# Optimization experiments

Measured on AMD Instinct MI355X. Metric: run time of the kernel, lower is better.

Reference implementation:

```python
import jax, jax.numpy as jnp
import numpy as np
import math

B, T, D_IN, D_OUT = 2, 2048, 4096, 4096
N_HEADS, N_KV = 32, 8
HEAD_DIM = D_OUT // N_HEADS  # 128
GROUP_SIZE = N_HEADS // N_KV  # 4
ROPE_BASE = 500000.0
CTX = 2048


def _rope_tables(head_dim, base, seq_len):
    inv_freq = 1.0 / base ** (jnp.arange(0, head_dim, 2, dtype=jnp.float32) / head_dim)
    t = jnp.arange(seq_len, dtype=jnp.float32)
    freqs = jnp.einsum('i,j->ij', t, inv_freq)  # (T, head_dim/2)
    return jnp.cos(freqs), jnp.sin(freqs)


def _apply_rope(x, cos, sin):
    # x: (B, H, T, Dh); cos/sin: (T, Dh/2)
    x1, x2 = jnp.split(x, 2, axis=-1)
    c = cos[None, None]
    s = sin[None, None]
    return jnp.concatenate([x1 * c - x2 * s, x1 * s + x2 * c], axis=-1)


def setup_inputs() -> dict:
    key = jax.random.key(0)
    ks = jax.random.split(key, 5)
    scale = 0.02
    return {
        'x': jax.random.normal(ks[0], (B, T, D_IN), dtype=jnp.float32),
        'Wq': jax.random.normal(ks[1], (D_IN, D_OUT), dtype=jnp.float32) * scale,
        'Wk': jax.random.normal(ks[2], (D_IN, N_KV * HEAD_DIM), dtype=jnp.float32) * scale,
        'Wv': jax.random.normal(ks[3], (D_IN, N_KV * HEAD_DIM), dtype=jnp.float32) * scale,
        'Wo': jax.random.normal(ks[4], (D_OUT, D_OUT), dtype=jnp.float32) * scale,
    }


def reference(x, Wq, Wk, Wv, Wo):
    b, t, _ = x.shape
    cos, sin = _rope_tables(HEAD_DIM, ROPE_BASE, t)  # start_pos = 0

    q = (x @ Wq).reshape(b, t, N_HEADS, HEAD_DIM).transpose(0, 2, 1, 3)  # (B,H,T,Dh)
    k = (x @ Wk).reshape(b, t, N_KV, HEAD_DIM).transpose(0, 2, 1, 3)    # (B,G,T,Dh)
    v = (x @ Wv).reshape(b, t, N_KV, HEAD_DIM).transpose(0, 2, 1, 3)    # (B,G,T,Dh)

    q = _apply_rope(q, cos, sin)
    k = _apply_rope(k, cos, sin)

    # GQA: repeat_interleave KV groups to match query heads
    k_h = jnp.repeat(k, GROUP_SIZE, axis=1)  # (B,H,T,Dh)
    v_h = jnp.repeat(v, GROUP_SIZE, axis=1)

    scores = jnp.einsum('bhqd,bhkd->bhqk', q, k_h) / math.sqrt(HEAD_DIM)
    causal = jnp.triu(jnp.ones((t, t), dtype=bool), k=1)
    scores = jnp.where(causal[None, None], jnp.finfo(scores.dtype).min, scores)
    attn = jax.nn.softmax(scores, axis=-1)

    ctx = jnp.einsum('bhqk,bhkd->bhqd', attn, v_h)           # (B,H,T,Dh)
    ctx = ctx.transpose(0, 2, 1, 3).reshape(b, t, D_OUT)     # (B,T,D)
    return ctx @ Wo
```

## Files before the change

kernel.cpp:

```cpp
#include <hip/hip_runtime.h>
#include <hip/hip_bf16.h>

#define T_SEQ 2048
#define NH 32
#define NKV 8
#define DH 128

typedef unsigned short u16;
typedef unsigned int u32;
typedef __attribute__((ext_vector_type(8))) short short8;
typedef __attribute__((ext_vector_type(4))) float floatx4;

union U8 { u16 s[8]; uint4 v; };
union F8 { u32 d[4]; short8 s; };

__device__ inline u16 f2bf(float f) {
  __hip_bfloat16 h = __float2bfloat16(f);
  return *reinterpret_cast<u16*>(&h);
}
__device__ inline float bf2f(u16 u) {
  __hip_bfloat16 h;
  *reinterpret_cast<u16*>(&h) = u;
  return __bfloat162float(h);
}

__device__ inline void store_out(float* p, float v) { *p = v; }
__device__ inline void store_out(u16* p, float v) { *p = f2bf(v); }

#define GLD_LDS(g, l) __builtin_amdgcn_global_load_lds( \
    (const __attribute__((address_space(1))) void*)(g), \
    (__attribute__((address_space(3))) void*)(l), 16, 0, 0)

__global__ void cast_x_kernel(const float* __restrict__ in, u16* __restrict__ out, int n8) {
  int idx = blockIdx.x * blockDim.x + threadIdx.x;
  if (idx >= n8) return;
  const float4* p = reinterpret_cast<const float4*>(in) + (size_t)idx * 2;
  float4 f0 = p[0], f1 = p[1];
  U8 u;
  u.s[0] = f2bf(f0.x); u.s[1] = f2bf(f0.y); u.s[2] = f2bf(f0.z); u.s[3] = f2bf(f0.w);
  u.s[4] = f2bf(f1.x); u.s[5] = f2bf(f1.y); u.s[6] = f2bf(f1.z); u.s[7] = f2bf(f1.w);
  *reinterpret_cast<uint4*>(out + (size_t)idx * 8) = u.v;
}

__global__ void transpose_cast_kernel(const float* __restrict__ W, u16* __restrict__ WT,
                                      int K, int N) {
  __shared__ u16 tile[64][72];
  int tid = threadIdx.x;
  int n0 = blockIdx.x * 64, k0 = blockIdx.y * 64;
  int r = tid >> 2, seg = (tid & 3) * 16;
  const float* wp = W + (size_t)(k0 + r) * N + n0 + seg;
#pragma unroll
  for (int jj = 0; jj < 4; ++jj) {
    float4 f = *(const float4*)(wp + jj * 4);
    tile[r][seg + jj * 4 + 0] = f2bf(f.x);
    tile[r][seg + jj * 4 + 1] = f2bf(f.y);
    tile[r][seg + jj * 4 + 2] = f2bf(f.z);
    tile[r][seg + jj * 4 + 3] = f2bf(f.w);
  }
  __syncthreads();
  u16* op = WT + (size_t)(n0 + r) * K + k0 + seg;
#pragma unroll
  for (int jj = 0; jj < 4; ++jj) {
    ushort4 o;
    o.x = tile[seg + jj * 4 + 0][r];
    o.y = tile[seg + jj * 4 + 1][r];
    o.z = tile[seg + jj * 4 + 2][r];
    o.w = tile[seg + jj * 4 + 3][r];
    *(ushort4*)(op + jj * 4) = o;
  }
}

__global__ void rope_kernel(u16* __restrict__ qkv) {
  int idx = blockIdx.x * blockDim.x + threadIdx.x;
  int i = idx & 63;
  int head = (idx >> 6) % 40;
  int row = idx / (64 * 40);
  int t = row & (T_SEQ - 1);
  int col = head < 32 ? head * 128 : 4096 + (head - 32) * 128;
  size_t base = (size_t)row * 6144 + col;
  float x1 = bf2f(qkv[base + i]);
  float x2 = bf2f(qkv[base + 64 + i]);
  float inv = exp2f(-(float)i * (18.931568569324174f / 64.0f));
  float ang = (float)t * inv;
  float c = cosf(ang), s = sinf(ang);
  qkv[base + i]      = f2bf(x1 * c - x2 * s);
  qkv[base + 64 + i] = f2bf(x1 * s + x2 * c);
}

__global__ void vtrans_kernel(const u16* __restrict__ qkv, u16* __restrict__ vt) {
  __shared__ u16 tile[64][72];
  int tid = threadIdx.x;
  int t0 = blockIdx.x * 64, d0 = blockIdx.y * 64, bg = blockIdx.z;
  int b = bg >> 3, g = bg & 7;
  int r = tid >> 2, seg = (tid & 3) * 16;
  const u16* src = qkv + (size_t)(b * T_SEQ + t0 + r) * 6144 + 5120 + g * 128 + d0 + seg;
  *(uint4*)&tile[r][seg] = *(const uint4*)src;
  *(uint4*)&tile[r][seg + 8] = *(const uint4*)(src + 8);
  __syncthreads();
  u16* dst = vt + (size_t)(bg * 128 + d0 + r) * T_SEQ + t0 + seg;
  U8 o0, o1;
#pragma unroll
  for (int e = 0; e < 8; ++e) o0.s[e] = tile[seg + e][r];
#pragma unroll
  for (int e = 0; e < 8; ++e) o1.s[e] = tile[seg + 8 + e][r];
  *(uint4*)dst = o0.v;
  *(uint4*)(dst + 8) = o1.v;
}

template <typename OutT>
__global__ __launch_bounds__(256) void gemm_bt(const u16* __restrict__ A,
                                               const u16* __restrict__ B,
                                               OutT* __restrict__ C,
                                               int M, int N, int Kd, int ldc) {
  __shared__ u16 As[128 * 64];
  __shared__ u16 Bs[128 * 64];
  int tid = threadIdx.x;
  int wave = tid >> 6, lane = tid & 63;
  int l15 = lane & 15, quad = lane >> 4;
  int wr = wave >> 1, wc = wave & 1;
  int m0 = blockIdx.y * 128, n0 = blockIdx.x * 128;

  floatx4 acc[4][4];
#pragma unroll
  for (int mt = 0; mt < 4; ++mt)
#pragma unroll
    for (int nt = 0; nt < 4; ++nt)
#pragma unroll
      for (int r = 0; r < 4; ++r) acc[mt][nt][r] = 0.0f;

  int rloc = lane >> 3, slot = lane & 7;
  const u16* agp = A + (size_t)(m0 + wave * 32 + rloc) * Kd + ((slot ^ rloc) * 8);
  const u16* bgp = B + (size_t)(n0 + wave * 32 + rloc) * Kd + ((slot ^ rloc) * 8);
  u16* alp = As + (wave * 32) * 64;
  u16* blp = Bs + (wave * 32) * 64;

  for (int kt = 0; kt < Kd; kt += 64) {
    __syncthreads();
#pragma unroll
    for (int j = 0; j < 4; ++j) {
      GLD_LDS(agp + kt + (size_t)j * 8 * Kd, alp + j * 8 * 64);
      GLD_LDS(bgp + kt + (size_t)j * 8 * Kd, blp + j * 8 * 64);
    }
    __syncthreads();
#pragma unroll
    for (int ks = 0; ks < 2; ++ks) {
      short8 af[4], bfr[4];
      int sl = ((ks * 4 + quad) ^ (l15 & 7)) * 8;
#pragma unroll
      for (int mt = 0; mt < 4; ++mt)
        af[mt] = *(const short8*)&As[(wr * 64 + mt * 16 + l15) * 64 + sl];
#pragma unroll
      for (int nt = 0; nt < 4; ++nt)
        bfr[nt] = *(const short8*)&Bs[(wc * 64 + nt * 16 + l15) * 64 + sl];
#pragma unroll
      for (int mt = 0; mt < 4; ++mt)
#pragma unroll
        for (int nt = 0; nt < 4; ++nt)
          acc[mt][nt] = __builtin_amdgcn_mfma_f32_16x16x32_bf16(af[mt], bfr[nt], acc[mt][nt], 0, 0, 0);
    }
  }

#pragma unroll
  for (int mt = 0; mt < 4; ++mt)
#pragma unroll
    for (int nt = 0; nt < 4; ++nt)
#pragma unroll
      for (int r = 0; r < 4; ++r) {
        int rr = m0 + wr * 64 + mt * 16 + quad * 4 + r;
        int cc = n0 + wc * 64 + nt * 16 + l15;
        store_out(&C[(size_t)rr * ldc + cc], acc[mt][nt][r]);
      }
}

__device__ inline void softmax_pv(floatx4* sc, float& m_s, float& ell_s,
                                  floatx4* o, const u16* Vsb,
                                  int qglob, int k0, bool diag,
                                  int l15, int quad) {
  const float scale = 0.08838834764831845f;
  float s[4][4];
#pragma unroll
  for (int t4 = 0; t4 < 4; ++t4)
#pragma unroll
    for (int r = 0; r < 4; ++r) {
      float v = sc[t4][r] * scale;
      if (diag && (k0 + t4 * 16 + quad * 4 + r > qglob)) v = -1e30f;
      s[t4][r] = v;
    }
  float m = s[0][0];
#pragma unroll
  for (int t4 = 0; t4 < 4; ++t4)
#pragma unroll
    for (int r = 0; r < 4; ++r) m = fmaxf(m, s[t4][r]);
  m = fmaxf(m, __shfl_xor(m, 16));
  m = fmaxf(m, __shfl_xor(m, 32));
  float mnew = fmaxf(m_s, m);
  float alpha = __expf(m_s - mnew);
  m_s = mnew;
  float sum = 0.f;
#pragma unroll
  for (int t4 = 0; t4 < 4; ++t4)
#pragma unroll
    for (int r = 0; r < 4; ++r) {
      float p = __expf(s[t4][r] - mnew);
      s[t4][r] = p;
      sum += p;
    }
  sum += __shfl_xor(sum, 16);
  sum += __shfl_xor(sum, 32);
  ell_s = ell_s * alpha + sum;
#pragma unroll
  for (int dt = 0; dt < 8; ++dt)
#pragma unroll
    for (int r = 0; r < 4; ++r) o[dt][r] *= alpha;

  u32 pk[4][2];
#pragma unroll
  for (int t4 = 0; t4 < 4; ++t4) {
    pk[t4][0] = (u32)f2bf(s[t4][0]) | ((u32)f2bf(s[t4][1]) << 16);
    pk[t4][1] = (u32)f2bf(s[t4][2]) | ((u32)f2bf(s[t4][3]) << 16);
  }
  int sidxA = (2 * (quad & 1)) * 16 + l15;
  int sidxB = sidxA + 16;
  bool hiq = (quad & 2) != 0;
  F8 pf[2];
#pragma unroll
  for (int h = 0; h < 2; ++h) {
    u32 a0 = __shfl((int)pk[2 * h][0], sidxA), b0 = __shfl((int)pk[2 * h + 1][0], sidxA);
    u32 a1 = __shfl((int)pk[2 * h][1], sidxA), b1 = __shfl((int)pk[2 * h + 1][1], sidxA);
    u32 a2 = __shfl((int)pk[2 * h][0], sidxB), b2 = __shfl((int)pk[2 * h + 1][0], sidxB);
    u32 a3 = __shfl((int)pk[2 * h][1], sidxB), b3 = __shfl((int)pk[2 * h + 1][1], sidxB);
    pf[h].d[0] = hiq ? b0 : a0;
    pf[h].d[1] = hiq ? b1 : a1;
    pf[h].d[2] = hiq ? b2 : a2;
    pf[h].d[3] = hiq ? b3 : a3;
  }
  int sl0 = ((0 + quad) ^ (l15 & 7)) * 8;
  int sl1 = ((4 + quad) ^ (l15 & 7)) * 8;
#pragma unroll
  for (int dt = 0; dt < 8; ++dt) {
    short8 va0 = *(const short8*)&Vsb[(dt * 16 + l15) * 64 + sl0];
    short8 va1 = *(const short8*)&Vsb[(dt * 16 + l15) * 64 + sl1];
    o[dt] = __builtin_amdgcn_mfma_f32_16x16x32_bf16(va0, pf[0].s, o[dt], 0, 0, 0);
    o[dt] = __builtin_amdgcn_mfma_f32_16x16x32_bf16(va1, pf[1].s, o[dt], 0, 0, 0);
  }
}

__global__ __launch_bounds__(256) void attn_kernel(const u16* __restrict__ qkv,
                                                   const u16* __restrict__ vt,
                                                   u16* __restrict__ CTX) {
  const int bx = blockIdx.x;
  const int bh = blockIdx.y;
  const int b = bh >> 5, h = bh & 31;
  const int g = h >> 2;
  const int bg = b * NKV + g;
  const int tid = threadIdx.x;
  const int w = tid >> 6, lane = tid & 63;
  const int l15 = lane & 15, quad = lane >> 4;
  const int lo = bx, hi = 31 - bx;
  const int niter = hi + 1;

  __shared__ u16 Ks[2 * 64 * 128];
  __shared__ u16 Vs[2 * 128 * 64];

  const u16* kbase = qkv + (size_t)(b * T_SEQ) * 6144 + 4096 + g * 128;
  const u16* vbase = vt + (size_t)(bg * 128) * T_SEQ;

  short8 aq[2][4];
  const int qg_lo = lo * 64 + w * 16 + l15;
  const int qg_hi = hi * 64 + w * 16 + l15;
  {
    const u16* qp0 = qkv + (size_t)(b * T_SEQ + qg_lo) * 6144 + h * 128;
    const u16* qp1 = qkv + (size_t)(b * T_SEQ + qg_hi) * 6144 + h * 128;
#pragma unroll
    for (int ks = 0; ks < 4; ++ks) {
      aq[0][ks] = *(const short8*)(qp0 + ks * 32 + quad * 8);
      aq[1][ks] = *(const short8*)(qp1 + ks * 32 + quad * 8);
    }
  }

  float m_s[2] = {-1e30f, -1e30f}, ell[2] = {0.f, 0.f};
  floatx4 o[2][8];
#pragma unroll
  for (int t = 0; t < 2; ++t)
#pragma unroll
    for (int dt = 0; dt < 8; ++dt)
#pragma unroll
      for (int r = 0; r < 4; ++r) o[t][dt][r] = 0.0f;

  const int krloc = lane >> 4, kslot = lane & 15;
  const int vrloc = lane >> 3, vslot = lane & 7;

  {
#pragma unroll
    for (int j = 0; j < 4; ++j) {
      int rk = w * 16 + j * 4 + krloc;
      int gck = (kslot & 8) | ((kslot & 7) ^ (rk & 7));
      GLD_LDS(kbase + (size_t)rk * 6144 + gck * 8, Ks + (w * 16 + j * 4) * 128);
      int rv = w * 32 + j * 8 + vrloc;
      int gcv = vslot ^ vrloc;
      GLD_LDS(vbase + (size_t)rv * 2048 + gcv * 8, Vs + (w * 32 + j * 8) * 64);
    }
  }

  for (int kt = 0; kt < niter; ++kt) {
    const int buf = kt & 1;
    const int k0 = kt * 64;
    __syncthreads();

    if (kt + 1 < niter) {
      const int nb = buf ^ 1;
      const int k0n = k0 + 64;
#pragma unroll
      for (int j = 0; j < 4; ++j) {
        int rk = w * 16 + j * 4 + krloc;
        int gck = (kslot & 8) | ((kslot & 7) ^ (rk & 7));
        GLD_LDS(kbase + (size_t)(k0n + rk) * 6144 + gck * 8,
                Ks + nb * 8192 + (w * 16 + j * 4) * 128);
        int rv = w * 32 + j * 8 + vrloc;
        int gcv = vslot ^ vrloc;
        GLD_LDS(vbase + (size_t)rv * 2048 + k0n + gcv * 8,
                Vs + nb * 8192 + (w * 32 + j * 8) * 64);
      }
    }

    const u16* Ksb = Ks + buf * 8192;
    const u16* Vsb = Vs + buf * 8192;
    const bool lo_on = (kt <= lo);

    floatx4 s0[4], s1[4];
#pragma unroll
    for (int t4 = 0; t4 < 4; ++t4)
#pragma unroll
      for (int r = 0; r < 4; ++r) { s0[t4][r] = 0.f; s1[t4][r] = 0.f; }

    if (lo_on) {
#pragma unroll
      for (int ks = 0; ks < 4; ++ks) {
        int c = ks * 4 + quad;
        int sl = ((c & 8) | ((c & 7) ^ (l15 & 7))) * 8;
#pragma unroll
        for (int t4 = 0; t4 < 4; ++t4) {
          short8 bk = *(const short8*)&Ksb[(t4 * 16 + l15) * 128 + sl];
          s1[t4] = __builtin_amdgcn_mfma_f32_16x16x32_bf16(bk, aq[1][ks], s1[t4], 0, 0, 0);
          s0[t4] = __builtin_amdgcn_mfma_f32_16x16x32_bf16(bk, aq[0][ks], s0[t4], 0, 0, 0);
        }
      }
    } else {
#pragma unroll
      for (int ks = 0; ks < 4; ++ks) {
        int c = ks * 4 + quad;
        int sl = ((c & 8) | ((c & 7) ^ (l15 & 7))) * 8;
#pragma unroll
        for (int t4 = 0; t4 < 4; ++t4) {
          short8 bk = *(const short8*)&Ksb[(t4 * 16 + l15) * 128 + sl];
          s1[t4] = __builtin_amdgcn_mfma_f32_16x16x32_bf16(bk, aq[1][ks], s1[t4], 0, 0, 0);
        }
      }
    }

    softmax_pv(s1, m_s[1], ell[1], o[1], Vsb, qg_hi, k0, kt == hi, l15, quad);
    if (lo_on)
      softmax_pv(s0, m_s[0], ell[0], o[0], Vsb, qg_lo, k0, kt == lo, l15, quad);
  }

#pragma unroll
  for (int t = 0; t < 2; ++t) {
    float inv_l = 1.0f / ell[t];
    int qglob = (t ? qg_hi : qg_lo);
    u16* cp = CTX + (size_t)(b * T_SEQ + qglob) * 4096 + h * 128 + quad * 4;
#pragma unroll
    for (int dt = 0; dt < 8; ++dt) {
      ushort4 pkd;
      pkd.x = f2bf(o[t][dt][0] * inv_l);
      pkd.y = f2bf(o[t][dt][1] * inv_l);
      pkd.z = f2bf(o[t][dt][2] * inv_l);
      pkd.w = f2bf(o[t][dt][3] * inv_l);
      *(ushort4*)(cp + dt * 16) = pkd;
    }
  }
}

extern "C" void kernel_launch(void* const* d_in, const int* in_sizes, int n_in,
                              void* d_out, int out_size, void* d_ws, size_t ws_size,
                              hipStream_t stream) {
  const float* x  = (const float*)d_in[0];
  const float* Wq = (const float*)d_in[1];
  const float* Wk = (const float*)d_in[2];
  const float* Wv = (const float*)d_in[3];
  const float* Wo = (const float*)d_in[4];
  float* out = (float*)d_out;

  char* ws = (char*)d_ws;
  const size_t SZ_X    = (size_t)4096 * 4096 * 2;
  const size_t SZ_QKVW = (size_t)6144 * 4096 * 2;
  u16* xb    = (u16*)(ws);
  u16* wqkvT = (u16*)(ws + SZ_X);
  u16* woT   = (u16*)(ws + SZ_X + SZ_QKVW);
  u16* qkv   = (u16*)(ws + SZ_X + SZ_QKVW + SZ_X);
  u16* vt    = (u16*)(ws + SZ_X + SZ_QKVW + SZ_X + SZ_QKVW);
  u16* ctx   = xb;

  cast_x_kernel<<<8192, 256, 0, stream>>>(x, xb, 2097152);
  transpose_cast_kernel<<<dim3(64, 64), 256, 0, stream>>>(Wq, wqkvT, 4096, 4096);
  transpose_cast_kernel<<<dim3(16, 64), 256, 0, stream>>>(Wk, wqkvT + (size_t)4096 * 4096, 4096, 1024);
  transpose_cast_kernel<<<dim3(16, 64), 256, 0, stream>>>(Wv, wqkvT + (size_t)5120 * 4096, 4096, 1024);
  transpose_cast_kernel<<<dim3(64, 64), 256, 0, stream>>>(Wo, woT, 4096, 4096);

  gemm_bt<u16><<<dim3(48, 32), 256, 0, stream>>>(xb, wqkvT, qkv, 4096, 6144, 4096, 6144);

  rope_kernel<<<40960, 256, 0, stream>>>(qkv);
  vtrans_kernel<<<dim3(32, 2, 16), 256, 0, stream>>>(qkv, vt);

  attn_kernel<<<dim3(16, 64), 256, 0, stream>>>(qkv, vt, ctx);

  gemm_bt<float><<<dim3(32, 32), 256, 0, stream>>>(ctx, woT, out, 4096, 4096, 4096, 4096);
}
```

Baseline: 929.0 us.

## Use exp2 softmax with lazy rescale, shared V loads and MFMA priority hints

Folds the 1/sqrt(d) scale and log2(e) into a single constant so exp2 with an FMA replaces expf. Skips rescaling the running output and sum unless the row maximum grows past a threshold (lazy rescaling). The PV step is pulled out of the softmax helper so that both query tiles share one set of V fragment loads from LDS. MFMA sections are wrapped in s_setprio raises to favour matrix work across waves. Lazy rescaling lets the stored max lag the true max, which risks precision if the threshold is too loose. Keeping both tiles' P fragments live at once also raises register pressure.

```diff
diff --git a/kernel.cpp b/kernel.cpp
--- a/kernel.cpp
+++ b/kernel.cpp
@@ -172,17 +172,17 @@
       }
 }
 
-__device__ inline void softmax_pv(floatx4* sc, float& m_s, float& ell_s,
-                                  floatx4* o, const u16* Vsb,
-                                  int qglob, int k0, bool diag,
-                                  int l15, int quad) {
-  const float scale = 0.08838834764831845f;
+__device__ inline void softmax_frags(floatx4* sc, float& m_s, float& ell_s,
+                                     floatx4* o, F8* pf,
+                                     int qglob, int k0, bool diag,
+                                     int l15, int quad) {
+  const float C = 0.12751553f;
   float s[4][4];
 #pragma unroll
   for (int t4 = 0; t4 < 4; ++t4)
 #pragma unroll
     for (int r = 0; r < 4; ++r) {
-      float v = sc[t4][r] * scale;
+      float v = sc[t4][r];
       if (diag && (k0 + t4 * 16 + quad * 4 + r > qglob)) v = -1e30f;
       s[t4][r] = v;
     }
@@ -193,25 +193,29 @@
     for (int r = 0; r < 4; ++r) m = fmaxf(m, s[t4][r]);
   m = fmaxf(m, __shfl_xor(m, 16));
   m = fmaxf(m, __shfl_xor(m, 32));
-  float mnew = fmaxf(m_s, m);
-  float alpha = __expf(m_s - mnew);
-  m_s = mnew;
+  if (!__all(m <= m_s + 90.5f)) {
+    float mnew = fmaxf(m_s, m);
+    float alpha = __builtin_amdgcn_exp2f((m_s - mnew) * C);
+    m_s = mnew;
+    ell_s *= alpha;
+#pragma unroll
+    for (int dt = 0; dt < 8; ++dt)
+#pragma unroll
+      for (int r = 0; r < 4; ++r) o[dt][r] *= alpha;
+  }
+  float mC = m_s * C;
   float sum = 0.f;
 #pragma unroll
   for (int t4 = 0; t4 < 4; ++t4)
 #pragma unroll
     for (int r = 0; r < 4; ++r) {
-      float p = __expf(s[t4][r] - mnew);
+      float p = __builtin_amdgcn_exp2f(__builtin_fmaf(s[t4][r], C, -mC));
       s[t4][r] = p;
       sum += p;
     }
   sum += __shfl_xor(sum, 16);
   sum += __shfl_xor(sum, 32);
-  ell_s = ell_s * alpha + sum;
-#pragma unroll
-  for (int dt = 0; dt < 8; ++dt)
-#pragma unroll
-    for (int r = 0; r < 4; ++r) o[dt][r] *= alpha;
+  ell_s += sum;
 
   u32 pk[4][2];
 #pragma unroll
@@ -222,7 +226,6 @@
   int sidxA = (2 * (quad & 1)) * 16 + l15;
   int sidxB = sidxA + 16;
   bool hiq = (quad & 2) != 0;
-  F8 pf[2];
 #pragma unroll
   for (int h = 0; h < 2; ++h) {
     u32 a0 = __shfl((int)pk[2 * h][0], sidxA), b0 = __shfl((int)pk[2 * h + 1][0], sidxA);
@@ -233,15 +236,6 @@
     pf[h].d[1] = hiq ? b1 : a1;
     pf[h].d[2] = hiq ? b2 : a2;
     pf[h].d[3] = hiq ? b3 : a3;
-  }
-  int sl0 = ((0 + quad) ^ (l15 & 7)) * 8;
-  int sl1 = ((4 + quad) ^ (l15 & 7)) * 8;
-#pragma unroll
-  for (int dt = 0; dt < 8; ++dt) {
-    short8 va0 = *(const short8*)&Vsb[(dt * 16 + l15) * 64 + sl0];
-    short8 va1 = *(const short8*)&Vsb[(dt * 16 + l15) * 64 + sl1];
-    o[dt] = __builtin_amdgcn_mfma_f32_16x16x32_bf16(va0, pf[0].s, o[dt], 0, 0, 0);
-    o[dt] = __builtin_amdgcn_mfma_f32_16x16x32_bf16(va1, pf[1].s, o[dt], 0, 0, 0);
   }
 }
 
@@ -333,6 +327,7 @@
 #pragma unroll
       for (int r = 0; r < 4; ++r) { s0[t4][r] = 0.f; s1[t4][r] = 0.f; }
 
+    __builtin_amdgcn_s_setprio(1);
     if (lo_on) {
 #pragma unroll
       for (int ks = 0; ks < 4; ++ks) {
@@ -357,10 +352,36 @@
         }
       }
     }
-
-    softmax_pv(s1, m_s[1], ell[1], o[1], Vsb, qg_hi, k0, kt == hi, l15, quad);
+    __builtin_amdgcn_s_setprio(0);
+
+    F8 pf1[2], pf0[2];
+    softmax_frags(s1, m_s[1], ell[1], o[1], pf1, qg_hi, k0, kt == hi, l15, quad);
     if (lo_on)
-      softmax_pv(s0, m_s[0], ell[0], o[0], Vsb, qg_lo, k0, kt == lo, l15, quad);
+      softmax_frags(s0, m_s[0], ell[0], o[0], pf0, qg_lo, k0, kt == lo, l15, quad);
+
+    int sl0 = ((0 + quad) ^ (l15 & 7)) * 8;
+    int sl1 = ((4 + quad) ^ (l15 & 7)) * 8;
+    __builtin_amdgcn_s_setprio(1);
+    if (lo_on) {
+#pragma unroll
+      for (int dt = 0; dt < 8; ++dt) {
+        short8 va0 = *(const short8*)&Vsb[(dt * 16 + l15) * 64 + sl0];
+        short8 va1 = *(const short8*)&Vsb[(dt * 16 + l15) * 64 + sl1];
+        o[1][dt] = __builtin_amdgcn_mfma_f32_16x16x32_bf16(va0, pf1[0].s, o[1][dt], 0, 0, 0);
+        o[1][dt] = __builtin_amdgcn_mfma_f32_16x16x32_bf16(va1, pf1[1].s, o[1][dt], 0, 0, 0);
+        o[0][dt] = __builtin_amdgcn_mfma_f32_16x16x32_bf16(va0, pf0[0].s, o[0][dt], 0, 0, 0);
+        o[0][dt] = __builtin_amdgcn_mfma_f32_16x16x32_bf16(va1, pf0[1].s, o[0][dt], 0, 0, 0);
+      }
+    } else {
+#pragma unroll
+      for (int dt = 0; dt < 8; ++dt) {
+        short8 va0 = *(const short8*)&Vsb[(dt * 16 + l15) * 64 + sl0];
+        short8 va1 = *(const short8*)&Vsb[(dt * 16 + l15) * 64 + sl1];
+        o[1][dt] = __builtin_amdgcn_mfma_f32_16x16x32_bf16(va0, pf1[0].s, o[1][dt], 0, 0, 0);
+        o[1][dt] = __builtin_amdgcn_mfma_f32_16x16x32_bf16(va1, pf1[1].s, o[1][dt], 0, 0, 0);
+      }
+    }
+    __builtin_amdgcn_s_setprio(0);
   }
 
 #pragma unroll
```

After: 945.6 us. No clear change (+1.8%).
